# Kernel optimization log

Hardware: AMD Instinct MI355X
Metric: run time of the kernel (lower is better)

Reference implementation:

```python
import jax, jax.numpy as jnp
import numpy as np

NUM_EMBEDDINGS = 1024
EMBEDDING_DIM = 64
COMMITMENT_COST = 0.25


def setup_inputs() -> dict:
    key = jax.random.key(0)
    k1, k2 = jax.random.split(key)
    inputs = jax.random.normal(k1, (64, 32, 32, EMBEDDING_DIM), dtype=jnp.float32)
    embeddings = jax.random.normal(k2, (NUM_EMBEDDINGS, EMBEDDING_DIM), dtype=jnp.float32)
    return {"inputs": inputs, "embeddings": embeddings}


def reference(inputs, embeddings):
    # flatten spatial dims: [B, HW, D]
    flat = jnp.reshape(inputs, (inputs.shape[0], -1, EMBEDDING_DIM))
    distances = (
        jnp.sum(flat ** 2, axis=2, keepdims=True)
        - 2.0 * jnp.einsum("btd,kd->btk", flat, embeddings)
        + jnp.sum(embeddings ** 2, axis=1)
    )
    encoding_indices = jnp.argmin(distances, axis=2)  # [B, HW]
    # direct gather == one-hot @ embeddings, same math, no [B,HW,K] one-hot
    quantized = jnp.take(embeddings, encoding_indices, axis=0)  # [B, HW, D]
    quantized = jnp.reshape(quantized, inputs.shape)
    e_latent_loss = jnp.mean((jax.lax.stop_gradient(quantized) - inputs) ** 2)
    loss = COMMITMENT_COST * e_latent_loss
    quantized = inputs + jax.lax.stop_gradient(quantized - inputs)
    return quantized, loss, encoding_indices
```

## Files before the change

### kernel.cpp

```cpp
#include <hip/hip_runtime.h>

#define D 64
#define NK 1024
#define QTOTAL 65536
#define NELEM (QTOTAL * D)
#define LOSS_OFF 4194304
#define IDX_OUT_OFF 4194305
#define CAPQ 16384
#define MARGIN 2.0e-3f

typedef float f32x16 __attribute__((ext_vector_type(16)));
typedef short bf16x8 __attribute__((ext_vector_type(8)));
typedef float f32x4 __attribute__((ext_vector_type(4)));
typedef unsigned int u32;
typedef unsigned short ushort_t;

#define WS_E2   0
#define WS_B    4096
#define WS_CNT  266240
#define WS_LIST 266496
#define WS_NEED 332032

__device__ __forceinline__ ushort_t f2bf(float f) {
    u32 u = __float_as_uint(f);
    return (ushort_t)((u + 0x7FFFu + ((u >> 16) & 1u)) >> 16);
}
__device__ __forceinline__ float bf2f(ushort_t h) {
    return __uint_as_float(((u32)h) << 16);
}

__global__ __launch_bounds__(256) void vqk0(const float* __restrict__ emb,
                                            u32* __restrict__ b32,
                                            float* __restrict__ e2, u32* __restrict__ cnt,
                                            float* __restrict__ out) {
    int gid = blockIdx.x * 256 + threadIdx.x;
    int c = gid >> 5;
    int d = (gid & 31) * 2;
    float2 v = ((const float2*)emb)[gid];
    ushort_t h0 = f2bf(v.x), h1 = f2bf(v.y);
    ushort_t m0 = f2bf(v.x - bf2f(h0)), m1 = f2bf(v.y - bf2f(h1));
    int t = c >> 4, row = c & 15;
    int g = (d & 31) >> 3;
    int bh = (d < 32) ? 0 : 1;
    int lane = g * 16 + row;
    int u = t * 1024 + lane * 4 + ((d & 7) >> 1);
    b32[u + bh * 256]       = (u32)h0 | ((u32)h1 << 16);
    b32[u + (bh + 2) * 256] = (u32)m0 | ((u32)m1 << 16);
    if (gid < NK) {
        const float4* e4 = (const float4*)(emb + (long)gid * D);
        float s = 0.f;
#pragma unroll
        for (int i = 0; i < D / 4; ++i) {
            float4 w = e4[i];
            s += w.x * w.x + w.y * w.y + w.z * w.z + w.w * w.w;
        }
        e2[gid] = s;
    }
    if (gid == 0) { out[LOSS_OFF] = 0.0f; *cnt = 0; }
}

#define COMPUTE_TILE(T, BH0, BH1, BM0, BM1) do {                               \
    const int c_ = (T) * 16 + row;                                             \
    const float h_ = e2l[c_];                                                  \
    _Pragma("unroll")                                                          \
    for (int s_ = 0; s_ < 2; ++s_) {                                           \
        f32x4 acc = {0.f, 0.f, 0.f, 0.f};                                      \
        acc = __builtin_amdgcn_mfma_f32_16x16x32_bf16(ah[s_][0], BM0, acc, 0, 0, 0); \
        acc = __builtin_amdgcn_mfma_f32_16x16x32_bf16(am[s_][0], BH0, acc, 0, 0, 0); \
        acc = __builtin_amdgcn_mfma_f32_16x16x32_bf16(ah[s_][0], BH0, acc, 0, 0, 0); \
        acc = __builtin_amdgcn_mfma_f32_16x16x32_bf16(ah[s_][1], BM1, acc, 0, 0, 0); \
        acc = __builtin_amdgcn_mfma_f32_16x16x32_bf16(am[s_][1], BH1, acc, 0, 0, 0); \
        acc = __builtin_amdgcn_mfma_f32_16x16x32_bf16(ah[s_][1], BH1, acc, 0, 0, 0); \
        _Pragma("unroll")                                                      \
        for (int r_ = 0; r_ < 4; ++r_) {                                       \
            int sl_ = s_ * 4 + r_;                                             \
            float sd_ = h_ - acc[r_];                                          \
            float ns2_ = fminf(fmaxf(sd_, s1v[sl_]), s2v[sl_]);      \
            bool lt_ = sd_ < s1v[sl_];                                         \
            i1v[sl_] = lt_ ? c_ : i1v[sl_];                                    \
            s1v[sl_] = fminf(sd_, s1v[sl_]);                                   \
            s2v[sl_] = ns2_;                                                   \
        }                                                                      \
    }                                                                          \
} while (0)

#define LDS_FRAG(SB, TT, H0, H1, M0, M1) do {                                  \
    const ushort_t* p_ = (SB) + (TT) * 2048 + l * 8;                           \
    H0 = *(const bf16x8*)(p_);                                                 \
    H1 = *(const bf16x8*)(p_ + 512);                                           \
    M0 = *(const bf16x8*)(p_ + 1024);                                          \
    M1 = *(const bf16x8*)(p_ + 1536);                                          \
} while (0)

__global__ __launch_bounds__(256, 2) void vqk1(const float* __restrict__ x,
                                               const ushort_t* __restrict__ B,
                                               const float* __restrict__ e2g,
                                               const float* __restrict__ emb,
                                               u32* __restrict__ cnt,
                                               int* __restrict__ list,
                                               float* __restrict__ out) {
    __shared__ f32x4 stage[2][1024];
    __shared__ float e2l[NK];
    __shared__ int   idx_l[128];
    __shared__ float lred[4];

    const int tid = threadIdx.x;
    const int l = tid & 63;
    const int w = tid >> 6;
    const int qbase = blockIdx.x * 128;
    const int wb = qbase + w * 32;
    const int row = l & 15;
    const int g = l >> 4;
    const int koff = g * 8;

    {
        f32x4 t = ((const f32x4*)e2g)[tid];
        ((f32x4*)e2l)[tid] = t * 0.5f;
    }

    bf16x8 ah[2][2], am[2][2];
#pragma unroll
    for (int s = 0; s < 2; ++s) {
        const float* xr = x + (long)(wb + s * 16 + row) * D + koff;
#pragma unroll
        for (int half = 0; half < 2; ++half) {
            float4 p0 = ((const float4*)(xr + half * 32))[0];
            float4 p1 = ((const float4*)(xr + half * 32))[1];
            float v[8] = {p0.x, p0.y, p0.z, p0.w, p1.x, p1.y, p1.z, p1.w};
#pragma unroll
            for (int i = 0; i < 8; ++i) {
                ushort_t hs = f2bf(v[i]);
                ushort_t ms = f2bf(v[i] - bf2f(hs));
                ah[s][half][i] = (short)hs;
                am[s][half][i] = (short)ms;
            }
        }
    }

    float s1v[8], s2v[8];
    int i1v[8];
#pragma unroll
    for (int i = 0; i < 8; ++i) { s1v[i] = 3.4e38f; s2v[i] = 3.4e38f; i1v[i] = 0; }

    const f32x4* gB = (const f32x4*)B;

    {
        f32x4 st0[4];
#pragma unroll
        for (int tt = 0; tt < 4; ++tt) st0[tt] = gB[tt * 256 + tid];
#pragma unroll
        for (int tt = 0; tt < 4; ++tt) stage[0][tt * 256 + tid] = st0[tt];
    }
    __syncthreads();

#pragma unroll 1
    for (int c = 0; c < 16; ++c) {
        const int cb = c & 1;
        const ushort_t* sb = (const ushort_t*)&stage[cb][0];

        f32x4 st[4];
        if (c < 15) {
#pragma unroll
            for (int tt = 0; tt < 4; ++tt)
                st[tt] = gB[(c + 1) * 1024 + tt * 256 + tid];
        }

        bf16x8 bh0, bh1, bm0, bm1, nh0, nh1, nm0, nm1;
        LDS_FRAG(sb, 0, bh0, bh1, bm0, bm1);
#pragma unroll
        for (int tt = 0; tt < 4; ++tt) {
            if (tt < 3) LDS_FRAG(sb, tt + 1, nh0, nh1, nm0, nm1);
            COMPUTE_TILE(c * 4 + tt, bh0, bh1, bm0, bm1);
            bh0 = nh0; bh1 = nh1; bm0 = nm0; bm1 = nm1;
        }

        if (c < 15) {
#pragma unroll
            for (int tt = 0; tt < 4; ++tt)
                stage[cb ^ 1][tt * 256 + tid] = st[tt];
        }
        __syncthreads();
    }

#pragma unroll
    for (int d = 1; d < 16; d <<= 1) {
#pragma unroll
        for (int sl = 0; sl < 8; ++sl) {
            float os1 = __shfl_xor(s1v[sl], d, 64);
            float os2 = __shfl_xor(s2v[sl], d, 64);
            int   oi1 = __shfl_xor(i1v[sl], d, 64);
            float hi = s1v[sl] > os1 ? s1v[sl] : os1;
            float lo2 = s2v[sl] < os2 ? s2v[sl] : os2;
            int ni = (os1 < s1v[sl]) ? oi1
                   : ((os1 == s1v[sl] && oi1 < i1v[sl]) ? oi1 : i1v[sl]);
            s1v[sl] = s1v[sl] < os1 ? s1v[sl] : os1;
            s2v[sl] = hi < lo2 ? hi : lo2;
            i1v[sl] = ni;
        }
    }

    if (row == 0) {
#pragma unroll
        for (int sl = 0; sl < 8; ++sl) {
            int s = sl >> 2, r = sl & 3;
            int ql = w * 32 + s * 16 + g * 4 + r;
            idx_l[ql] = i1v[sl];
            if (s2v[sl] - s1v[sl] <= MARGIN) {
                u32 p = atomicAdd(cnt, 1u);
                if (p < CAPQ) list[p] = qbase + ql;
            }
        }
    }
    __syncthreads();

    if (l < 32) out[IDX_OUT_OFF + wb + l] = (float)idx_l[w * 32 + l];

    const f32x4* x4 = (const f32x4*)(x + (long)wb * D);
    const f32x4* e4 = (const f32x4*)emb;
    f32x4* o4 = (f32x4*)(out + (long)wb * D);
    float ls = 0.f;
#pragma unroll 1
    for (int k = 0; k < 8; ++k) {
        int j = l + 64 * k;
        int ql = j >> 4;
        int col = j & 15;
        int idx = idx_l[w * 32 + ql];
        f32x4 xv = x4[j];
        f32x4 ev = e4[idx * 16 + col];
        o4[j] = ev;
        f32x4 dd = ev - xv;
        ls += dd[0] * dd[0] + dd[1] * dd[1] + dd[2] * dd[2] + dd[3] * dd[3];
    }
#pragma unroll
    for (int offr = 32; offr > 0; offr >>= 1) ls += __shfl_down(ls, offr, 64);
    if (l == 0) lred[w] = ls;
    __syncthreads();
    if (tid == 0)
        atomicAdd(&out[LOSS_OFF],
                  (lred[0] + lred[1] + lred[2] + lred[3]) * (0.25f / (float)NELEM));
}

__global__ __launch_bounds__(64) void vqk2(const float* __restrict__ x,
                                           const float* __restrict__ emb,
                                           const float* __restrict__ e2,
                                           const int* __restrict__ list,
                                           const u32* __restrict__ cnt,
                                           float* __restrict__ out) {
    u32 n = *cnt; if (n > CAPQ) n = CAPQ;
    const int l = threadIdx.x;
    for (u32 f = blockIdx.x; f < n; f += gridDim.x) {
        int q = list[f];
        float4 xv[16];
        const float4* xp = (const float4*)(x + (long)q * D);
#pragma unroll
        for (int i = 0; i < 16; ++i) xv[i] = xp[i];
        float best = 3.4e38f; int bi = 0;
#pragma unroll 1
        for (int i = 0; i < 16; ++i) {
            int c = l * 16 + i;
            const float4* ep = (const float4*)(emb + (long)c * D);
            float a0 = 0.f, a1 = 0.f, a2 = 0.f, a3 = 0.f;
#pragma unroll
            for (int k = 0; k < 16; ++k) {
                float4 e = ep[k];
                a0 = fmaf(e.x, xv[k].x, a0); a1 = fmaf(e.y, xv[k].y, a1);
                a2 = fmaf(e.z, xv[k].z, a2); a3 = fmaf(e.w, xv[k].w, a3);
            }
            float s = 0.5f * e2[c] - ((a0 + a1) + (a2 + a3));
            if (s < best) { best = s; bi = c; }
        }
#pragma unroll
        for (int off = 32; off > 0; off >>= 1) {
            float ob = __shfl_down(best, off, 64);
            int   oi = __shfl_down(bi, off, 64);
            if (ob < best || (ob == best && oi < bi)) { best = ob; bi = oi; }
        }
        bi = __shfl(bi, 0, 64);
        int ci = (int)out[IDX_OUT_OFF + q];
        if (bi != ci) {
            float xl = x[(long)q * D + l];
            float en = emb[(long)bi * D + l];
            float eo = emb[(long)ci * D + l];
            out[(long)q * D + l] = en;
            float dn = (en - xl) * (en - xl);
            float dol = (eo - xl) * (eo - xl);
            float dd = dn - dol;
#pragma unroll
            for (int off = 32; off > 0; off >>= 1) dd += __shfl_down(dd, off, 64);
            if (l == 0) {
                out[IDX_OUT_OFF + q] = (float)bi;
                atomicAdd(&out[LOSS_OFF], dd * (0.25f / (float)NELEM));
            }
        }
    }
}

#define FDO_CHUNK(B, K) \
    aA0 = fmaf(B[0],  xA[4*K+0].x, aA0); aA1 = fmaf(B[1],  xA[4*K+0].y, aA1); \
    aA2 = fmaf(B[2],  xA[4*K+0].z, aA2); aA3 = fmaf(B[3],  xA[4*K+0].w, aA3); \
    aA0 = fmaf(B[4],  xA[4*K+1].x, aA0); aA1 = fmaf(B[5],  xA[4*K+1].y, aA1); \
    aA2 = fmaf(B[6],  xA[4*K+1].z, aA2); aA3 = fmaf(B[7],  xA[4*K+1].w, aA3); \
    aA0 = fmaf(B[8],  xA[4*K+2].x, aA0); aA1 = fmaf(B[9],  xA[4*K+2].y, aA1); \
    aA2 = fmaf(B[10], xA[4*K+2].z, aA2); aA3 = fmaf(B[11], xA[4*K+2].w, aA3); \
    aA0 = fmaf(B[12], xA[4*K+3].x, aA0); aA1 = fmaf(B[13], xA[4*K+3].y, aA1); \
    aA2 = fmaf(B[14], xA[4*K+3].z, aA2); aA3 = fmaf(B[15], xA[4*K+3].w, aA3); \
    aB0 = fmaf(B[0],  xB[4*K+0].x, aB0); aB1 = fmaf(B[1],  xB[4*K+0].y, aB1); \
    aB2 = fmaf(B[2],  xB[4*K+0].z, aB2); aB3 = fmaf(B[3],  xB[4*K+0].w, aB3); \
    aB0 = fmaf(B[4],  xB[4*K+1].x, aB0); aB1 = fmaf(B[5],  xB[4*K+1].y, aB1); \
    aB2 = fmaf(B[6],  xB[4*K+1].z, aB2); aB3 = fmaf(B[7],  xB[4*K+1].w, aB3); \
    aB0 = fmaf(B[8],  xB[4*K+2].x, aB0); aB1 = fmaf(B[9],  xB[4*K+2].y, aB1); \
    aB2 = fmaf(B[10], xB[4*K+2].z, aB2); aB3 = fmaf(B[11], xB[4*K+2].w, aB3); \
    aB0 = fmaf(B[12], xB[4*K+3].x, aB0); aB1 = fmaf(B[13], xB[4*K+3].y, aB1); \
    aB2 = fmaf(B[14], xB[4*K+3].z, aB2); aB3 = fmaf(B[15], xB[4*K+3].w, aB3);

__global__ __launch_bounds__(256) void vq_e2f(const float* __restrict__ emb,
                                              float* __restrict__ e2,
                                              float* __restrict__ out) {
    int k = blockIdx.x * blockDim.x + threadIdx.x;
    if (k == 0) out[LOSS_OFF] = 0.0f;
    if (k < NK) {
        const float4* e4 = (const float4*)(emb + k * D);
        float s = 0.f;
#pragma unroll
        for (int i = 0; i < D / 4; ++i) {
            float4 v = e4[i];
            s += v.x * v.x + v.y * v.y + v.z * v.z + v.w * v.w;
        }
        e2[k] = s;
    }
}

__global__ __launch_bounds__(256, 2) void vq_mainf(const float* __restrict__ x,
                                                   const float* __restrict__ emb,
                                                   const float* __restrict__ e2g,
                                                   float* __restrict__ out) {
    __shared__ float e2l[NK];
    __shared__ float sm_s[512];
    __shared__ int   sm_c[512];
    const int tid = threadIdx.x;
    const int l = tid & 63;
    const int w = tid >> 6;
    const int qbase = blockIdx.x * 128;
    ((float4*)e2l)[tid] = ((const float4*)e2g)[tid];
    float4 xA[16], xB[16];
    const float4* xpA = (const float4*)(x + (long)(qbase + l) * D);
    const float4* xpB = (const float4*)(x + (long)(qbase + 64 + l) * D);
#pragma unroll
    for (int i = 0; i < 16; ++i) { xA[i] = xpA[i]; xB[i] = xpB[i]; }
    __syncthreads();
    const int code0 = __builtin_amdgcn_readfirstlane(w << 8);
    const float* ep0 = emb + (long)code0 * D;
    float bestA = 3.4e38f, bestB = 3.4e38f;
    int idxA = 0, idxB = 0;
#pragma unroll 1
    for (int g = 0; g < 256; ++g) {
        const float* ep = ep0 + g * D;
        f32x16 b0, b1, b2, b3;
        asm volatile(
            "s_load_dwordx16 %0, %4, 0x0\n\t"
            "s_load_dwordx16 %1, %4, 0x40\n\t"
            "s_load_dwordx16 %2, %4, 0x80\n\t"
            "s_load_dwordx16 %3, %4, 0xC0\n\t"
            "s_waitcnt lgkmcnt(0)"
            : "=s"(b0), "=s"(b1), "=s"(b2), "=s"(b3) : "s"(ep));
        float aA0 = 0.f, aA1 = 0.f, aA2 = 0.f, aA3 = 0.f;
        float aB0 = 0.f, aB1 = 0.f, aB2 = 0.f, aB3 = 0.f;
        FDO_CHUNK(b0, 0) FDO_CHUNK(b1, 1) FDO_CHUNK(b2, 2) FDO_CHUNK(b3, 3)
        float dotA = (aA0 + aA1) + (aA2 + aA3);
        float dotB = (aB0 + aB1) + (aB2 + aB3);
        float e2c = e2l[code0 + g];
        float sA = 0.5f * e2c - dotA;
        float sB = 0.5f * e2c - dotB;
        int code = code0 + g;
        bool lt;
        lt = sA < bestA; bestA = lt ? sA : bestA; idxA = lt ? code : idxA;
        lt = sB < bestB; bestB = lt ? sB : bestB; idxB = lt ? code : idxB;
    }
    sm_s[w * 128 + l] = bestA;      sm_c[w * 128 + l] = idxA;
    sm_s[w * 128 + 64 + l] = bestB; sm_c[w * 128 + 64 + l] = idxB;
    __syncthreads();
    if (tid < 128) {
        float bs = sm_s[tid]; int bc = sm_c[tid];
#pragma unroll
        for (int wv = 1; wv < 4; ++wv) {
            float s = sm_s[wv * 128 + tid]; int c = sm_c[wv * 128 + tid];
            if (s < bs) { bs = s; bc = c; }
        }
        const int q = qbase + tid;
        out[IDX_OUT_OFF + q] = (float)bc;
        const float4* eb = (const float4*)(emb + (long)bc * D);
        const float4* xq = (const float4*)(x + (long)q * D);
        float4* oq = (float4*)(out + (long)q * D);
        float lsum = 0.f;
#pragma unroll
        for (int i = 0; i < 16; ++i) {
            float4 e = eb[i]; float4 xx = xq[i];
            oq[i] = e;
            float dx = e.x - xx.x, dy = e.y - xx.y, dz = e.z - xx.z, dw = e.w - xx.w;
            lsum += dx * dx + dy * dy + dz * dz + dw * dw;
        }
#pragma unroll
        for (int o = 32; o > 0; o >>= 1) lsum += __shfl_down(lsum, o, 64);
        if ((tid & 63) == 0) atomicAdd(&out[LOSS_OFF], lsum * (0.25f / (float)NELEM));
    }
}

extern "C" void kernel_launch(void* const* d_in, const int* in_sizes, int n_in,
                              void* d_out, int out_size, void* d_ws, size_t ws_size,
                              hipStream_t stream) {
    const float* x   = (const float*)d_in[0];
    const float* emb = (const float*)d_in[1];
    float* out = (float*)d_out;
    char* ws = (char*)d_ws;

    if (ws_size < (size_t)WS_NEED) {
        float* e2 = (float*)ws;
        vq_e2f<<<4, 256, 0, stream>>>(emb, e2, out);
        vq_mainf<<<QTOTAL / 128, 256, 0, stream>>>(x, emb, e2, out);
        return;
    }

    float* e2    = (float*)(ws + WS_E2);
    ushort_t* B  = (ushort_t*)(ws + WS_B);
    u32* cnt     = (u32*)(ws + WS_CNT);
    int* list    = (int*)(ws + WS_LIST);

    vqk0<<<128, 256, 0, stream>>>(emb, (u32*)B, e2, cnt, out);
    vqk1<<<QTOTAL / 128, 256, 0, stream>>>(x, B, e2, emb, cnt, list, out);
    vqk2<<<256, 64, 0, stream>>>(x, emb, e2, list, cnt, out);
}
```

Baseline: 121.7 us.

## Use 8 waves per block with 16 queries each in VQ distance kernel

The main kernel moves from 4 waves each handling 32 queries to 8 waves each handling 16 queries, with 512 threads per block. The codebook stage chunk doubles to 128 codes, so there are 8 pipeline iterations instead of 16. Each wave now holds half the query fragments and running-min state, which frees registers for higher occupancy (launch bounds 512,4). In exchange, every codebook fragment read from LDS is reused by only one query tile instead of two, which doubles LDS read traffic per MFMA, and the staging LDS footprint doubles.

```diff
diff --git a/kernel.cpp b/kernel.cpp
--- a/kernel.cpp
+++ b/kernel.cpp
@@ -12,6 +12,7 @@
 typedef float f32x16 __attribute__((ext_vector_type(16)));
 typedef short bf16x8 __attribute__((ext_vector_type(8)));
 typedef float f32x4 __attribute__((ext_vector_type(4)));
+typedef float f32x2 __attribute__((ext_vector_type(2)));
 typedef unsigned int u32;
 typedef unsigned short ushort_t;
 
@@ -62,25 +63,21 @@
 #define COMPUTE_TILE(T, BH0, BH1, BM0, BM1) do {                               \
     const int c_ = (T) * 16 + row;                                             \
     const float h_ = e2l[c_];                                                  \
+    f32x4 acc = {0.f, 0.f, 0.f, 0.f};                                          \
+    acc = __builtin_amdgcn_mfma_f32_16x16x32_bf16(ah[0], BM0, acc, 0, 0, 0);   \
+    acc = __builtin_amdgcn_mfma_f32_16x16x32_bf16(am[0], BH0, acc, 0, 0, 0);   \
+    acc = __builtin_amdgcn_mfma_f32_16x16x32_bf16(ah[0], BH0, acc, 0, 0, 0);   \
+    acc = __builtin_amdgcn_mfma_f32_16x16x32_bf16(ah[1], BM1, acc, 0, 0, 0);   \
+    acc = __builtin_amdgcn_mfma_f32_16x16x32_bf16(am[1], BH1, acc, 0, 0, 0);   \
+    acc = __builtin_amdgcn_mfma_f32_16x16x32_bf16(ah[1], BH1, acc, 0, 0, 0);   \
     _Pragma("unroll")                                                          \
-    for (int s_ = 0; s_ < 2; ++s_) {                                           \
-        f32x4 acc = {0.f, 0.f, 0.f, 0.f};                                      \
-        acc = __builtin_amdgcn_mfma_f32_16x16x32_bf16(ah[s_][0], BM0, acc, 0, 0, 0); \
-        acc = __builtin_amdgcn_mfma_f32_16x16x32_bf16(am[s_][0], BH0, acc, 0, 0, 0); \
-        acc = __builtin_amdgcn_mfma_f32_16x16x32_bf16(ah[s_][0], BH0, acc, 0, 0, 0); \
-        acc = __builtin_amdgcn_mfma_f32_16x16x32_bf16(ah[s_][1], BM1, acc, 0, 0, 0); \
-        acc = __builtin_amdgcn_mfma_f32_16x16x32_bf16(am[s_][1], BH1, acc, 0, 0, 0); \
-        acc = __builtin_amdgcn_mfma_f32_16x16x32_bf16(ah[s_][1], BH1, acc, 0, 0, 0); \
-        _Pragma("unroll")                                                      \
-        for (int r_ = 0; r_ < 4; ++r_) {                                       \
-            int sl_ = s_ * 4 + r_;                                             \
-            float sd_ = h_ - acc[r_];                                          \
-            float ns2_ = fminf(fmaxf(sd_, s1v[sl_]), s2v[sl_]);      \
-            bool lt_ = sd_ < s1v[sl_];                                         \
-            i1v[sl_] = lt_ ? c_ : i1v[sl_];                                    \
-            s1v[sl_] = fminf(sd_, s1v[sl_]);                                   \
-            s2v[sl_] = ns2_;                                                   \
-        }                                                                      \
+    for (int r_ = 0; r_ < 4; ++r_) {                                           \
+        float sd_ = h_ - acc[r_];                                              \
+        float ns2_ = fminf(fmaxf(sd_, s1v[r_]), s2v[r_]);            \
+        bool lt_ = sd_ < s1v[r_];                                              \
+        i1v[r_] = lt_ ? c_ : i1v[r_];                                          \
+        s1v[r_] = fminf(sd_, s1v[r_]);                                         \
+        s2v[r_] = ns2_;                                                        \
     }                                                                          \
 } while (0)
 
@@ -92,36 +89,35 @@
     M1 = *(const bf16x8*)(p_ + 1536);                                          \
 } while (0)
 
-__global__ __launch_bounds__(256, 2) void vqk1(const float* __restrict__ x,
+__global__ __launch_bounds__(512, 4) void vqk1(const float* __restrict__ x,
                                                const ushort_t* __restrict__ B,
                                                const float* __restrict__ e2g,
                                                const float* __restrict__ emb,
                                                u32* __restrict__ cnt,
                                                int* __restrict__ list,
                                                float* __restrict__ out) {
-    __shared__ f32x4 stage[2][1024];
+    __shared__ f32x4 stage[2][2048];
     __shared__ float e2l[NK];
     __shared__ int   idx_l[128];
-    __shared__ float lred[4];
+    __shared__ float lred[8];
 
     const int tid = threadIdx.x;
     const int l = tid & 63;
     const int w = tid >> 6;
     const int qbase = blockIdx.x * 128;
-    const int wb = qbase + w * 32;
+    const int wb = qbase + w * 16;
     const int row = l & 15;
     const int g = l >> 4;
     const int koff = g * 8;
 
     {
-        f32x4 t = ((const f32x4*)e2g)[tid];
-        ((f32x4*)e2l)[tid] = t * 0.5f;
-    }
-
-    bf16x8 ah[2][2], am[2][2];
-#pragma unroll
-    for (int s = 0; s < 2; ++s) {
-        const float* xr = x + (long)(wb + s * 16 + row) * D + koff;
+        f32x2 t = ((const f32x2*)e2g)[tid];
+        ((f32x2*)e2l)[tid] = t * 0.5f;
+    }
+
+    bf16x8 ah[2], am[2];
+    {
+        const float* xr = x + (long)(wb + row) * D + koff;
 #pragma unroll
         for (int half = 0; half < 2; ++half) {
             float4 p0 = ((const float4*)(xr + half * 32))[0];
@@ -131,53 +127,53 @@
             for (int i = 0; i < 8; ++i) {
                 ushort_t hs = f2bf(v[i]);
                 ushort_t ms = f2bf(v[i] - bf2f(hs));
-                ah[s][half][i] = (short)hs;
-                am[s][half][i] = (short)ms;
+                ah[half][i] = (short)hs;
+                am[half][i] = (short)ms;
             }
         }
     }
 
-    float s1v[8], s2v[8];
-    int i1v[8];
-#pragma unroll
-    for (int i = 0; i < 8; ++i) { s1v[i] = 3.4e38f; s2v[i] = 3.4e38f; i1v[i] = 0; }
+    float s1v[4], s2v[4];
+    int i1v[4];
+#pragma unroll
+    for (int i = 0; i < 4; ++i) { s1v[i] = 3.4e38f; s2v[i] = 3.4e38f; i1v[i] = 0; }
 
     const f32x4* gB = (const f32x4*)B;
 
     {
         f32x4 st0[4];
 #pragma unroll
-        for (int tt = 0; tt < 4; ++tt) st0[tt] = gB[tt * 256 + tid];
-#pragma unroll
-        for (int tt = 0; tt < 4; ++tt) stage[0][tt * 256 + tid] = st0[tt];
+        for (int tt = 0; tt < 4; ++tt) st0[tt] = gB[tt * 512 + tid];
+#pragma unroll
+        for (int tt = 0; tt < 4; ++tt) stage[0][tt * 512 + tid] = st0[tt];
     }
     __syncthreads();
 
 #pragma unroll 1
-    for (int c = 0; c < 16; ++c) {
+    for (int c = 0; c < 8; ++c) {
         const int cb = c & 1;
         const ushort_t* sb = (const ushort_t*)&stage[cb][0];
 
         f32x4 st[4];
-        if (c < 15) {
+        if (c < 7) {
 #pragma unroll
             for (int tt = 0; tt < 4; ++tt)
-                st[tt] = gB[(c + 1) * 1024 + tt * 256 + tid];
+                st[tt] = gB[(c + 1) * 2048 + tt * 512 + tid];
         }
 
         bf16x8 bh0, bh1, bm0, bm1, nh0, nh1, nm0, nm1;
         LDS_FRAG(sb, 0, bh0, bh1, bm0, bm1);
 #pragma unroll
-        for (int tt = 0; tt < 4; ++tt) {
-            if (tt < 3) LDS_FRAG(sb, tt + 1, nh0, nh1, nm0, nm1);
-            COMPUTE_TILE(c * 4 + tt, bh0, bh1, bm0, bm1);
+        for (int tt = 0; tt < 8; ++tt) {
+            if (tt < 7) LDS_FRAG(sb, tt + 1, nh0, nh1, nm0, nm1);
+            COMPUTE_TILE(c * 8 + tt, bh0, bh1, bm0, bm1);
             bh0 = nh0; bh1 = nh1; bm0 = nm0; bm1 = nm1;
         }
 
-        if (c < 15) {
+        if (c < 7) {
 #pragma unroll
             for (int tt = 0; tt < 4; ++tt)
-                stage[cb ^ 1][tt * 256 + tid] = st[tt];
+                stage[cb ^ 1][tt * 512 + tid] = st[tt];
         }
         __syncthreads();
     }
@@ -185,7 +181,7 @@
 #pragma unroll
     for (int d = 1; d < 16; d <<= 1) {
 #pragma unroll
-        for (int sl = 0; sl < 8; ++sl) {
+        for (int sl = 0; sl < 4; ++sl) {
             float os1 = __shfl_xor(s1v[sl], d, 64);
             float os2 = __shfl_xor(s2v[sl], d, 64);
             int   oi1 = __shfl_xor(i1v[sl], d, 64);
@@ -201,9 +197,8 @@
 
     if (row == 0) {
 #pragma unroll
-        for (int sl = 0; sl < 8; ++sl) {
-            int s = sl >> 2, r = sl & 3;
-            int ql = w * 32 + s * 16 + g * 4 + r;
+        for (int sl = 0; sl < 4; ++sl) {
+            int ql = w * 16 + g * 4 + sl;
             idx_l[ql] = i1v[sl];
             if (s2v[sl] - s1v[sl] <= MARGIN) {
                 u32 p = atomicAdd(cnt, 1u);
@@ -213,18 +208,18 @@
     }
     __syncthreads();
 
-    if (l < 32) out[IDX_OUT_OFF + wb + l] = (float)idx_l[w * 32 + l];
+    if (l < 16) out[IDX_OUT_OFF + wb + l] = (float)idx_l[w * 16 + l];
 
     const f32x4* x4 = (const f32x4*)(x + (long)wb * D);
     const f32x4* e4 = (const f32x4*)emb;
     f32x4* o4 = (f32x4*)(out + (long)wb * D);
     float ls = 0.f;
 #pragma unroll 1
-    for (int k = 0; k < 8; ++k) {
+    for (int k = 0; k < 4; ++k) {
         int j = l + 64 * k;
         int ql = j >> 4;
         int col = j & 15;
-        int idx = idx_l[w * 32 + ql];
+        int idx = idx_l[w * 16 + ql];
         f32x4 xv = x4[j];
         f32x4 ev = e4[idx * 16 + col];
         o4[j] = ev;
@@ -235,9 +230,12 @@
     for (int offr = 32; offr > 0; offr >>= 1) ls += __shfl_down(ls, offr, 64);
     if (l == 0) lred[w] = ls;
     __syncthreads();
-    if (tid == 0)
-        atomicAdd(&out[LOSS_OFF],
-                  (lred[0] + lred[1] + lred[2] + lred[3]) * (0.25f / (float)NELEM));
+    if (tid == 0) {
+        float t = 0.f;
+#pragma unroll
+        for (int i = 0; i < 8; ++i) t += lred[i];
+        atomicAdd(&out[LOSS_OFF], t * (0.25f / (float)NELEM));
+    }
 }
 
 __global__ __launch_bounds__(64) void vqk2(const float* __restrict__ x,
@@ -426,6 +424,6 @@
     int* list    = (int*)(ws + WS_LIST);
 
     vqk0<<<128, 256, 0, stream>>>(emb, (u32*)B, e2, cnt, out);
-    vqk1<<<QTOTAL / 128, 256, 0, stream>>>(x, B, e2, emb, cnt, list, out);
+    vqk1<<<QTOTAL / 128, 512, 0, stream>>>(x, B, e2, emb, cnt, list, out);
     vqk2<<<256, 64, 0, stream>>>(x, emb, e2, list, cnt, out);
 }
```

Result: no change. 121.0 us, median of 2 (-0.6%).

## Load codebook fragments directly from global memory and raise MFMA wave priority

Applied to the files above, without the earlier changes.

Drops the double-buffered LDS staging of the bf16 codebook. Each wave now loads its MFMA B fragments straight from global memory (L2-resident) into registers, with a two-tile register prefetch and no per-chunk __syncthreads. It also wraps the MFMA tile compute in s_setprio to favour waves that are issuing matrix ops. This removes the LDS write/read traffic and the barriers, but each wave now repeats the global fragment loads, adding L2 traffic and load latency that the prefetch has to hide.

```diff
diff --git a/kernel.cpp b/kernel.cpp
--- a/kernel.cpp
+++ b/kernel.cpp
@@ -62,6 +62,7 @@
 #define COMPUTE_TILE(T, BH0, BH1, BM0, BM1) do {                               \
     const int c_ = (T) * 16 + row;                                             \
     const float h_ = e2l[c_];                                                  \
+    __builtin_amdgcn_s_setprio(1);                                             \
     _Pragma("unroll")                                                          \
     for (int s_ = 0; s_ < 2; ++s_) {                                           \
         f32x4 acc = {0.f, 0.f, 0.f, 0.f};                                      \
@@ -82,10 +83,11 @@
             s2v[sl_] = ns2_;                                                   \
         }                                                                      \
     }                                                                          \
+    __builtin_amdgcn_s_setprio(0);                                             \
 } while (0)
 
-#define LDS_FRAG(SB, TT, H0, H1, M0, M1) do {                                  \
-    const ushort_t* p_ = (SB) + (TT) * 2048 + l * 8;                           \
+#define GLB_FRAG(T, H0, H1, M0, M1) do {                                       \
+    const ushort_t* p_ = B + (T) * 2048 + l * 8;                               \
     H0 = *(const bf16x8*)(p_);                                                 \
     H1 = *(const bf16x8*)(p_ + 512);                                           \
     M0 = *(const bf16x8*)(p_ + 1024);                                          \
@@ -99,7 +101,6 @@
                                                u32* __restrict__ cnt,
                                                int* __restrict__ list,
                                                float* __restrict__ out) {
-    __shared__ f32x4 stage[2][1024];
     __shared__ float e2l[NK];
     __shared__ int   idx_l[128];
     __shared__ float lred[4];
@@ -142,45 +143,20 @@
 #pragma unroll
     for (int i = 0; i < 8; ++i) { s1v[i] = 3.4e38f; s2v[i] = 3.4e38f; i1v[i] = 0; }
 
-    const f32x4* gB = (const f32x4*)B;
-
-    {
-        f32x4 st0[4];
-#pragma unroll
-        for (int tt = 0; tt < 4; ++tt) st0[tt] = gB[tt * 256 + tid];
-#pragma unroll
-        for (int tt = 0; tt < 4; ++tt) stage[0][tt * 256 + tid] = st0[tt];
-    }
     __syncthreads();
 
+    bf16x8 fa0, fa1, fa2, fa3, fb0, fb1, fb2, fb3;
+    GLB_FRAG(0, fa0, fa1, fa2, fa3);
+    GLB_FRAG(1, fb0, fb1, fb2, fb3);
 #pragma unroll 1
-    for (int c = 0; c < 16; ++c) {
-        const int cb = c & 1;
-        const ushort_t* sb = (const ushort_t*)&stage[cb][0];
-
-        f32x4 st[4];
-        if (c < 15) {
-#pragma unroll
-            for (int tt = 0; tt < 4; ++tt)
-                st[tt] = gB[(c + 1) * 1024 + tt * 256 + tid];
-        }
-
-        bf16x8 bh0, bh1, bm0, bm1, nh0, nh1, nm0, nm1;
-        LDS_FRAG(sb, 0, bh0, bh1, bm0, bm1);
-#pragma unroll
-        for (int tt = 0; tt < 4; ++tt) {
-            if (tt < 3) LDS_FRAG(sb, tt + 1, nh0, nh1, nm0, nm1);
-            COMPUTE_TILE(c * 4 + tt, bh0, bh1, bm0, bm1);
-            bh0 = nh0; bh1 = nh1; bm0 = nm0; bm1 = nm1;
-        }
-
-        if (c < 15) {
-#pragma unroll
-            for (int tt = 0; tt < 4; ++tt)
-                stage[cb ^ 1][tt * 256 + tid] = st[tt];
-        }
-        __syncthreads();
-    }
+    for (int t = 0; t < 62; t += 2) {
+        COMPUTE_TILE(t, fa0, fa1, fa2, fa3);
+        GLB_FRAG(t + 2, fa0, fa1, fa2, fa3);
+        COMPUTE_TILE(t + 1, fb0, fb1, fb2, fb3);
+        GLB_FRAG(t + 3, fb0, fb1, fb2, fb3);
+    }
+    COMPUTE_TILE(62, fa0, fa1, fa2, fa3);
+    COMPUTE_TILE(63, fb0, fb1, fb2, fb3);
 
 #pragma unroll
     for (int d = 1; d < 16; d <<= 1) {
```

Result: no change. 121.9 us (+0.1%).
